# Optimization experiments

Measured on AMD Instinct MI355X. Metric: run time of the kernel, lower is better.

The kernel has to match this reference:

```python
import jax, jax.numpy as jnp
import numpy as np
import math

EMBED_DIM = 1024
N_HEADS = 16
HEAD_DIM = EMBED_DIM // N_HEADS
B, N = 2, 2048


def setup_inputs() -> dict:
    key = jax.random.key(0)
    k1, k2, k3 = jax.random.split(key, 3)
    x = jax.random.normal(k1, (B, N, EMBED_DIM), dtype=jnp.float32)
    # Per-head Linear(D, 3*head_dim), stacked over heads. PyTorch Linear init scale ~1/sqrt(fan_in).
    bound = 1.0 / math.sqrt(EMBED_DIM)
    Wkqv = jax.random.uniform(k2, (N_HEADS, EMBED_DIM, 3 * HEAD_DIM), dtype=jnp.float32, minval=-bound, maxval=bound)
    bkqv = jax.random.uniform(k3, (N_HEADS, 3 * HEAD_DIM), dtype=jnp.float32, minval=-bound, maxval=bound)
    return {"x": x, "Wkqv": Wkqv, "bkqv": bkqv}


def reference(x, Wkqv, bkqv):
    Bx, Nx, D = x.shape
    hd = Wkqv.shape[-1] // 3
    # all heads at once: [B, H, N, 3*hd]
    proj = jnp.einsum('bnd,hdf->bhnf', x, Wkqv) + bkqv[None, :, None, :]
    # torch.split order in the original is (k, q, v)
    k, q, v = jnp.split(proj, 3, axis=-1)
    # scores = q @ k^T / sqrt(head_dim)   [B, H, N, N]
    scores = jnp.einsum('bhqd,bhkd->bhqk', q, k) / math.sqrt(hd)
    causal = jnp.tril(jnp.ones((Nx, Nx), dtype=bool))
    scores = jnp.where(causal[None, None, :, :], scores, -jnp.inf)
    attn = jax.nn.softmax(scores, axis=-1)
    out = jnp.einsum('bhqk,bhkd->bhqd', attn, v)  # [B, H, N, hd]
    # concat heads -> [B, N, D]  (forward() passes no out_matrix, so no output projection)
    return out.transpose(0, 2, 1, 3).reshape(Bx, Nx, D)
```

## Files before the change

kernel.cpp:

```cpp
#include <hip/hip_runtime.h>
#include <math.h>

typedef float f32x4 __attribute__((ext_vector_type(4)));
typedef __bf16 bf16x8 __attribute__((ext_vector_type(8)));

#define MFMA16(a, b, c) __builtin_amdgcn_mfma_f32_16x16x32_bf16((a), (b), (c), 0, 0, 0)

constexpr int Bsz = 2, Nseq = 2048, Dm = 1024, Hh = 16, HDim = 64, F3 = 192;
constexpr int Mrows = Bsz * Nseq;
constexpr int NC = Hh * F3;
constexpr float QSCALE = 0.125f * 1.4426950408889634f;

__device__ inline void load_lds16(const void* g, void* l) {
    __builtin_amdgcn_global_load_lds((const __attribute__((address_space(1))) void*)g,
                                     (__attribute__((address_space(3))) void*)l, 16, 0, 0);
}

__global__ __launch_bounds__(256) void conv_x_kernel(const float* __restrict__ x,
                                                     __bf16* __restrict__ xb) {
    int i = blockIdx.x * 256 + threadIdx.x;
    const float4* xv = reinterpret_cast<const float4*>(x);
    float4 a = xv[2 * i];
    float4 b = xv[2 * i + 1];
    bf16x8 o = {(__bf16)a.x, (__bf16)a.y, (__bf16)a.z, (__bf16)a.w,
                (__bf16)b.x, (__bf16)b.y, (__bf16)b.z, (__bf16)b.w};
    *reinterpret_cast<bf16x8*>(xb + 8 * i) = o;
}

__global__ __launch_bounds__(256) void conv_w_kernel(const float* __restrict__ w,
                                                     __bf16* __restrict__ wt) {
    __shared__ __bf16 tile[32][66];
    int h = blockIdx.z, d0 = blockIdx.x * 32, c0 = blockIdx.y * 64;
    for (int i = threadIdx.x; i < 32 * 64; i += 256) {
        int di = i >> 6, cj = i & 63;
        tile[di][cj] = (__bf16)w[(size_t)(h * Dm + d0 + di) * F3 + c0 + cj];
    }
    __syncthreads();
    for (int i = threadIdx.x; i < 32 * 64; i += 256) {
        int ci = i >> 5, dj = i & 31;
        wt[(size_t)(h * F3 + c0 + ci) * Dm + d0 + dj] = tile[dj][ci];
    }
}

__global__ __launch_bounds__(512, 2) void gemm_proj(const __bf16* __restrict__ xb,
                                                    const __bf16* __restrict__ wt,
                                                    const float* __restrict__ bias,
                                                    __bf16* __restrict__ kbuf,
                                                    __bf16* __restrict__ qbuf,
                                                    __bf16* __restrict__ vt) {
    __shared__ __align__(16) __bf16 Ab[2][256 * 64];
    __shared__ __align__(16) __bf16 Bb[2][256 * 64];

    int flat = blockIdx.x;
    int swz = (flat & 7) * 24 + (flat >> 3);
    int bm = swz / 12, bn = swz % 12;
    int r0 = bm * 256, n0 = bn * 256;

    int w = threadIdx.x >> 6, lane = threadIdx.x & 63;
    int col = lane & 15, quad = lane >> 4;
    int wm = w >> 2, wn = w & 3;

    f32x4 acc[8][4] = {};

    auto stage = [&](int kt, int s) {
        int rbase = w * 32;
        int rl = lane >> 3;
        int cg = ((lane & 7) ^ rl) * 8;
#pragma unroll
        for (int i = 0; i < 4; i++) {
            int row = rbase + i * 8 + rl;
            load_lds16(xb + (size_t)(r0 + row) * Dm + kt * 64 + cg,
                       &Ab[s][(rbase + i * 8) * 64]);
            load_lds16(wt + (size_t)(n0 + row) * Dm + kt * 64 + cg,
                       &Bb[s][(rbase + i * 8) * 64]);
        }
    };

    stage(0, 0);
    stage(1, 1);

    for (int j = 0; j < 16; j++) {
        int s = j & 1;
        if (j < 15) asm volatile("s_waitcnt vmcnt(8)" ::: "memory");
        else        asm volatile("s_waitcnt vmcnt(0)" ::: "memory");
        __builtin_amdgcn_s_barrier();
        asm volatile("" ::: "memory");

#pragma unroll
        for (int ks = 0; ks < 2; ks++) {
            int cq = ks * 4 + quad;
            bf16x8 af[8], bfr[4];
#pragma unroll
            for (int mt = 0; mt < 8; mt++) {
                int row = wm * 128 + mt * 16 + col;
                af[mt] = *reinterpret_cast<const bf16x8*>(
                    &Ab[s][row * 64 + ((cq ^ (row & 7)) * 8)]);
            }
#pragma unroll
            for (int nt = 0; nt < 4; nt++) {
                int row = wn * 64 + nt * 16 + col;
                bfr[nt] = *reinterpret_cast<const bf16x8*>(
                    &Bb[s][row * 64 + ((cq ^ (row & 7)) * 8)]);
            }
            __builtin_amdgcn_s_setprio(1);
#pragma unroll
            for (int mt = 0; mt < 8; mt++)
#pragma unroll
                for (int nt = 0; nt < 4; nt++)
                    acc[mt][nt] = MFMA16(af[mt], bfr[nt], acc[mt][nt]);
            __builtin_amdgcn_s_setprio(0);
        }

        asm volatile("" ::: "memory");
        __builtin_amdgcn_s_barrier();
        asm volatile("" ::: "memory");
        if (j + 2 < 16) stage(j + 2, s);
    }

#pragma unroll
    for (int nt = 0; nt < 4; nt++) {
        int g = n0 + wn * 64 + nt * 16 + col;
        int h = g / F3, c = g - h * F3;
        float bv = bias[g];
        bool isq = (c >= 64 && c < 128), isv = (c >= 128);
        int cd = c & 63;
#pragma unroll
        for (int mt = 0; mt < 8; mt++) {
#pragma unroll
            for (int rg = 0; rg < 4; rg++) {
                int r = r0 + wm * 128 + mt * 16 + quad * 4 + rg;
                int b = r >> 11, n = r & (Nseq - 1);
                float v = acc[mt][nt][rg] + bv;
                if (isq) v *= QSCALE;
                size_t bh = (size_t)(b * Hh + h);
                if (isv) vt[(bh * HDim + cd) * Nseq + n] = (__bf16)v;
                else ((isq) ? qbuf : kbuf)[(bh * Nseq + n) * HDim + cd] = (__bf16)v;
            }
        }
    }
}

__global__ __launch_bounds__(256) void proj_small(const float* __restrict__ x,
                                                  const __bf16* __restrict__ wt,
                                                  const float* __restrict__ bias,
                                                  __bf16* __restrict__ kbuf,
                                                  __bf16* __restrict__ qbuf,
                                                  __bf16* __restrict__ vt) {
    int h = blockIdx.y;
    int wave = threadIdx.x >> 6, lane = threadIdx.x & 63;
    int col = lane & 15, quad = lane >> 4;
    int r0 = blockIdx.x * 128 + wave * 32;

    f32x4 acc[12][2] = {};
    const float* xr0 = x + (size_t)(r0 + col) * Dm + quad * 8;
    const float* xr1 = xr0 + 16 * Dm;
    const __bf16* wbase = wt + (size_t)(h * F3 + col) * Dm + quad * 8;

    for (int k0 = 0; k0 < Dm; k0 += 32) {
        float4 a0lo = *reinterpret_cast<const float4*>(xr0 + k0);
        float4 a0hi = *reinterpret_cast<const float4*>(xr0 + k0 + 4);
        float4 a1lo = *reinterpret_cast<const float4*>(xr1 + k0);
        float4 a1hi = *reinterpret_cast<const float4*>(xr1 + k0 + 4);
        bf16x8 a0 = {(__bf16)a0lo.x, (__bf16)a0lo.y, (__bf16)a0lo.z, (__bf16)a0lo.w,
                     (__bf16)a0hi.x, (__bf16)a0hi.y, (__bf16)a0hi.z, (__bf16)a0hi.w};
        bf16x8 a1 = {(__bf16)a1lo.x, (__bf16)a1lo.y, (__bf16)a1lo.z, (__bf16)a1lo.w,
                     (__bf16)a1hi.x, (__bf16)a1hi.y, (__bf16)a1hi.z, (__bf16)a1hi.w};
#pragma unroll
        for (int ct = 0; ct < 12; ct++) {
            bf16x8 bf = *reinterpret_cast<const bf16x8*>(wbase + ct * 16 * Dm + k0);
            acc[ct][0] = MFMA16(a0, bf, acc[ct][0]);
            acc[ct][1] = MFMA16(a1, bf, acc[ct][1]);
        }
    }
#pragma unroll
    for (int ct = 0; ct < 12; ct++) {
        int c = ct * 16 + col;
        float bv = bias[h * F3 + c];
        int cd = c & 63;
        bool isq = (c >= 64 && c < 128), isv = (c >= 128);
#pragma unroll
        for (int rt = 0; rt < 2; rt++) {
#pragma unroll
            for (int rg = 0; rg < 4; rg++) {
                int r = r0 + rt * 16 + quad * 4 + rg;
                int b = r >> 11, n = r & (Nseq - 1);
                float v = acc[ct][rt][rg] + bv;
                if (isq) v *= QSCALE;
                size_t bh = (size_t)(b * Hh + h);
                if (isv) vt[(bh * HDim + cd) * Nseq + n] = (__bf16)v;
                else ((isq) ? qbuf : kbuf)[(bh * Nseq + n) * HDim + cd] = (__bf16)v;
            }
        }
    }
}

__global__ __launch_bounds__(512) void attn_kernel(const __bf16* __restrict__ qbuf,
                                                   const __bf16* __restrict__ kbuf,
                                                   const __bf16* __restrict__ vt,
                                                   float* __restrict__ out) {
    __shared__ __align__(16) __bf16 Kb[64 * 64];
    __shared__ __align__(16) __bf16 Vb[64 * 64];
    __shared__ __align__(16) __bf16 plds[8][16][72];
    int bh = blockIdx.x;
    int b = bh >> 4, h = bh & 15;
    int pair = blockIdx.y;
    int wave = threadIdx.x >> 6, lane = threadIdx.x & 63;
    int col = lane & 15, quad = lane >> 4;
    int tile = (wave < 4) ? pair : (31 - pair);
    int q0 = tile * 64 + (wave & 3) * 16;

    const __bf16* qbase = qbuf + (size_t)bh * Nseq * HDim;
    const __bf16* kbase = kbuf + (size_t)bh * Nseq * HDim;
    const __bf16* vbase = vt + (size_t)bh * HDim * Nseq;

    bf16x8 aq0 = *reinterpret_cast<const bf16x8*>(qbase + (q0 + col) * HDim + quad * 8);
    bf16x8 aq1 = *reinterpret_cast<const bf16x8*>(qbase + (q0 + col) * HDim + quad * 8 + 32);

    f32x4 o[4] = {};
    float lsum[4] = {0.f, 0.f, 0.f, 0.f};

    int mb = q0 & ~63;
    int loop_end = 2048 - 64 * pair;

    int srow = threadIdx.x >> 3;
    int schunk = (threadIdx.x & 7) ^ (srow & 7);
    const __bf16* ksrc0 = kbase + srow * HDim + schunk * 8;
    const __bf16* vsrc0 = vbase + (size_t)srow * Nseq + schunk * 8;
    __bf16* kdst = Kb + wave * 512;
    __bf16* vdst = Vb + wave * 512;

    int sw0 = ((quad ^ (col & 7)) * 8);
    int sw1 = (((quad + 4) ^ (col & 7)) * 8);

    for (int kb = 0; kb < loop_end; kb += 64) {
        __syncthreads();
        load_lds16(ksrc0 + kb * HDim, kdst);
        load_lds16(vsrc0 + kb, vdst);
        __syncthreads();

        if (kb <= mb) {
            bool masked = (kb == mb);
            f32x4 z = {};
            f32x4 s[4];
#pragma unroll
            for (int g = 0; g < 4; g++) {
                const __bf16* krow = Kb + (col + 16 * g) * 64;
                bf16x8 k0 = *reinterpret_cast<const bf16x8*>(krow + sw0);
                bf16x8 k1 = *reinterpret_cast<const bf16x8*>(krow + sw1);
                s[g] = MFMA16(aq0, k0, z);
                s[g] = MFMA16(aq1, k1, s[g]);
            }
            if (masked) {
#pragma unroll
                for (int g = 0; g < 4; g++) {
#pragma unroll
                    for (int r = 0; r < 4; r++) {
                        int qi = q0 + quad * 4 + r;
                        float p = (kb + col + 16 * g <= qi) ? exp2f(s[g][r]) : 0.f;
                        lsum[r] += p;
                        plds[wave][quad * 4 + r][col + 16 * g] = (__bf16)p;
                    }
                }
            } else {
#pragma unroll
                for (int g = 0; g < 4; g++) {
#pragma unroll
                    for (int r = 0; r < 4; r++) {
                        float p = exp2f(s[g][r]);
                        lsum[r] += p;
                        plds[wave][quad * 4 + r][col + 16 * g] = (__bf16)p;
                    }
                }
            }
            bf16x8 pa0 = *reinterpret_cast<const bf16x8*>(&plds[wave][col][quad * 8]);
            bf16x8 pa1 = *reinterpret_cast<const bf16x8*>(&plds[wave][col][32 + quad * 8]);
#pragma unroll
            for (int nt = 0; nt < 4; nt++) {
                const __bf16* vrow = Vb + (col + 16 * nt) * 64;
                bf16x8 v0 = *reinterpret_cast<const bf16x8*>(vrow + sw0);
                bf16x8 v1 = *reinterpret_cast<const bf16x8*>(vrow + sw1);
                o[nt] = MFMA16(pa0, v0, o[nt]);
                o[nt] = MFMA16(pa1, v1, o[nt]);
            }
        }
    }

    float linv[4];
#pragma unroll
    for (int r = 0; r < 4; r++) {
        float s = lsum[r];
        s += __shfl_xor(s, 1);
        s += __shfl_xor(s, 2);
        s += __shfl_xor(s, 4);
        s += __shfl_xor(s, 8);
        linv[r] = 1.f / s;
    }
#pragma unroll
    for (int nt = 0; nt < 4; nt++) {
#pragma unroll
        for (int r = 0; r < 4; r++) {
            int qi = q0 + quad * 4 + r;
            out[((size_t)(b * Nseq + qi)) * Dm + h * HDim + nt * 16 + col] = o[nt][r] * linv[r];
        }
    }
}

extern "C" void kernel_launch(void* const* d_in, const int* in_sizes, int n_in,
                              void* d_out, int out_size, void* d_ws, size_t ws_size,
                              hipStream_t stream) {
    const float* x = nullptr;
    const float* w = nullptr;
    const float* bias = nullptr;
    for (int i = 0; i < n_in; i++) {
        if (in_sizes[i] == Mrows * Dm) x = (const float*)d_in[i];
        else if (in_sizes[i] == Hh * Dm * F3) w = (const float*)d_in[i];
        else if (in_sizes[i] == Hh * F3) bias = (const float*)d_in[i];
    }
    float* outp = (float*)d_out;

    char* ws = (char*)d_ws;
    __bf16* wt = (__bf16*)(ws);
    __bf16* kbuf = (__bf16*)(ws + 6291456);
    __bf16* qbuf = (__bf16*)(ws + 6291456 + 8388608);
    __bf16* vt = (__bf16*)(ws + 6291456 + 2 * 8388608);
    __bf16* xb = (__bf16*)(ws + 6291456 + 3 * 8388608);

    conv_w_kernel<<<dim3(Dm / 32, F3 / 64, Hh), 256, 0, stream>>>(w, wt);
    if (ws_size >= (size_t)(6291456 + 4 * 8388608)) {
        conv_x_kernel<<<Mrows * Dm / (8 * 256), 256, 0, stream>>>(x, xb);
        gemm_proj<<<dim3(Mrows / 256 * (NC / 256)), 512, 0, stream>>>(xb, wt, bias, kbuf, qbuf, vt);
    } else {
        proj_small<<<dim3(Mrows / 128, Hh), 256, 0, stream>>>(x, wt, bias, kbuf, qbuf, vt);
    }
    attn_kernel<<<dim3(32, 16), 512, 0, stream>>>(qbuf, kbuf, vt, outp);
}
```

Baseline: 169.6 us.

## Restructure QKV projection GEMM main loop into quarter-tile interleaved load/compute schedule

Replaces the simple double-buffered K-loop of the QKV projection GEMM with a finer-grained 8-phase schedule. The 256x256 tile is split into half-tiles of A and B, and their global-to-LDS loads are interleaved between quarter-tile MFMA blocks, with barriers around each block. The goal is to overlap memory traffic with MFMA work more evenly and to reduce register pressure by holding fewer fragments at once. The cost is many more barriers per iteration and more complex buffer-reuse ordering, which could cause stalls or races if the waitcnt accounting is wrong.

```diff
diff --git a/kernel.cpp b/kernel.cpp
--- a/kernel.cpp
+++ b/kernel.cpp
@@ -15,6 +15,10 @@
     __builtin_amdgcn_global_load_lds((const __attribute__((address_space(1))) void*)g,
                                      (__attribute__((address_space(3))) void*)l, 16, 0, 0);
 }
+
+#define FENCE asm volatile("" ::: "memory")
+#define BARRIER do { FENCE; __builtin_amdgcn_s_barrier(); FENCE; } while (0)
+#define WAIT6 asm volatile("s_waitcnt vmcnt(6)" ::: "memory")
 
 __global__ __launch_bounds__(256) void conv_x_kernel(const float* __restrict__ x,
                                                      __bf16* __restrict__ xb) {
@@ -61,60 +65,105 @@
     int wm = w >> 2, wn = w & 3;
 
     f32x4 acc[8][4] = {};
-
-    auto stage = [&](int kt, int s) {
-        int rbase = w * 32;
+    bf16x8 af[2][4];
+    bf16x8 bfr[2][2];
+
+    auto stageA = [&](int t, int s, int h) {
         int rl = lane >> 3;
-        int cg = ((lane & 7) ^ rl) * 8;
-#pragma unroll
-        for (int i = 0; i < 4; i++) {
-            int row = rbase + i * 8 + rl;
-            load_lds16(xb + (size_t)(r0 + row) * Dm + kt * 64 + cg,
-                       &Ab[s][(rbase + i * 8) * 64]);
-            load_lds16(wt + (size_t)(n0 + row) * Dm + kt * 64 + cg,
-                       &Bb[s][(rbase + i * 8) * 64]);
-        }
-    };
-
-    stage(0, 0);
-    stage(1, 1);
-
-    for (int j = 0; j < 16; j++) {
-        int s = j & 1;
-        if (j < 15) asm volatile("s_waitcnt vmcnt(8)" ::: "memory");
-        else        asm volatile("s_waitcnt vmcnt(0)" ::: "memory");
-        __builtin_amdgcn_s_barrier();
-        asm volatile("" ::: "memory");
-
-#pragma unroll
-        for (int ks = 0; ks < 2; ks++) {
-            int cq = ks * 4 + quad;
-            bf16x8 af[8], bfr[4];
-#pragma unroll
-            for (int mt = 0; mt < 8; mt++) {
-                int row = wm * 128 + mt * 16 + col;
-                af[mt] = *reinterpret_cast<const bf16x8*>(
-                    &Ab[s][row * 64 + ((cq ^ (row & 7)) * 8)]);
-            }
-#pragma unroll
-            for (int nt = 0; nt < 4; nt++) {
-                int row = wn * 64 + nt * 16 + col;
-                bfr[nt] = *reinterpret_cast<const bf16x8*>(
-                    &Bb[s][row * 64 + ((cq ^ (row & 7)) * 8)]);
-            }
-            __builtin_amdgcn_s_setprio(1);
-#pragma unroll
-            for (int mt = 0; mt < 8; mt++)
-#pragma unroll
-                for (int nt = 0; nt < 4; nt++)
-                    acc[mt][nt] = MFMA16(af[mt], bfr[nt], acc[mt][nt]);
-            __builtin_amdgcn_s_setprio(0);
-        }
-
-        asm volatile("" ::: "memory");
-        __builtin_amdgcn_s_barrier();
-        asm volatile("" ::: "memory");
-        if (j + 2 < 16) stage(j + 2, s);
+        int cg = (lane & 7) ^ rl;
+#pragma unroll
+        for (int r = 0; r < 2; r++) {
+            int rowb = r * 128 + h * 64 + w * 8;
+            load_lds16(xb + (size_t)(r0 + rowb + rl) * Dm + t * 64 + cg * 8,
+                       &Ab[s][rowb * 64]);
+        }
+    };
+    auto stageB = [&](int t, int s, int h) {
+        int rl = lane >> 3;
+        int cg = (lane & 7) ^ rl;
+#pragma unroll
+        for (int r = 0; r < 2; r++) {
+            int rowb = ((w >> 2) + r * 2) * 64 + h * 32 + (w & 3) * 8;
+            load_lds16(wt + (size_t)(n0 + rowb + rl) * Dm + t * 64 + cg * 8,
+                       &Bb[s][rowb * 64]);
+        }
+    };
+
+    auto readA = [&](int s, int mh) {
+#pragma unroll
+        for (int ks = 0; ks < 2; ks++)
+#pragma unroll
+            for (int mt = 0; mt < 4; mt++) {
+                int row = wm * 128 + mh * 64 + mt * 16 + col;
+                af[ks][mt] = *reinterpret_cast<const bf16x8*>(
+                    &Ab[s][row * 64 + (((ks * 4 + quad) ^ (row & 7)) * 8)]);
+            }
+    };
+    auto readB = [&](int s, int nh) {
+#pragma unroll
+        for (int ks = 0; ks < 2; ks++)
+#pragma unroll
+            for (int nt = 0; nt < 2; nt++) {
+                int row = wn * 64 + nh * 32 + nt * 16 + col;
+                bfr[ks][nt] = *reinterpret_cast<const bf16x8*>(
+                    &Bb[s][row * 64 + (((ks * 4 + quad) ^ (row & 7)) * 8)]);
+            }
+    };
+    auto mfmaQ = [&](int mh, int nh) {
+        __builtin_amdgcn_s_setprio(1);
+#pragma unroll
+        for (int ks = 0; ks < 2; ks++)
+#pragma unroll
+            for (int mt = 0; mt < 4; mt++)
+#pragma unroll
+                for (int nt = 0; nt < 2; nt++)
+                    acc[mh * 4 + mt][nh * 2 + nt] =
+                        MFMA16(af[ks][mt], bfr[ks][nt], acc[mh * 4 + mt][nh * 2 + nt]);
+        __builtin_amdgcn_s_setprio(0);
+    };
+
+    stageA(0, 0, 0); stageB(0, 0, 0); stageA(0, 0, 1); stageB(0, 0, 1);
+    stageA(1, 1, 0);
+    stageB(1, 1, 0); stageA(1, 1, 1);
+    WAIT6;
+    BARRIER;
+
+    for (int i = 0; i < 8; i++) {
+        int t0 = 2 * i;
+        int t2 = t0 + 2; if (t2 > 15) t2 = 15;
+        int t3 = t0 + 3; if (t3 > 15) t3 = 15;
+
+        readA(0, 0); readB(0, 0);
+        stageB(t0 + 1, 1, 1);
+        BARRIER; mfmaQ(0, 0); BARRIER;
+
+        readB(0, 1);
+        stageA(t2, 0, 0);
+        BARRIER; mfmaQ(0, 1); BARRIER;
+
+        readA(0, 1); readB(0, 0);
+        BARRIER; mfmaQ(1, 0); BARRIER;
+
+        readB(0, 1);
+        stageB(t2, 0, 0); stageA(t2, 0, 1);
+        WAIT6;
+        BARRIER; mfmaQ(1, 1); BARRIER;
+
+        readA(1, 0); readB(1, 0);
+        stageB(t2, 0, 1);
+        BARRIER; mfmaQ(0, 0); BARRIER;
+
+        readB(1, 1);
+        stageA(t3, 1, 0);
+        BARRIER; mfmaQ(0, 1); BARRIER;
+
+        readA(1, 1); readB(1, 0);
+        BARRIER; mfmaQ(1, 0); BARRIER;
+
+        readB(1, 1);
+        stageB(t3, 1, 0); stageA(t3, 1, 1);
+        WAIT6;
+        BARRIER; mfmaQ(1, 1); BARRIER;
     }
 
 #pragma unroll
```

After: 172.0 us. About the same (+1.4%).

## Retile projection GEMM to 256x192 and double-buffer attention K/V with per-tile blocks

Applied to the files above, without the earlier changes.

The projection GEMM moves from 256x256 to 256x192 output tiles, giving 256 blocks instead of 192 to fill the CUs better. The attention kernel stops pairing a short and a long query tile in one 512-thread block. It now launches one 256-thread block per 64-row query tile, heaviest tiles first, and double-buffers K/V loads into LDS so the next block's load overlaps compute. The risks are more blocks, load imbalance across the causal triangle, and lower MFMA reuse per B-fragment in the GEMM.

```diff
diff --git a/kernel.cpp b/kernel.cpp
--- a/kernel.cpp
+++ b/kernel.cpp
@@ -15,6 +15,9 @@
     __builtin_amdgcn_global_load_lds((const __attribute__((address_space(1))) void*)g,
                                      (__attribute__((address_space(3))) void*)l, 16, 0, 0);
 }
+
+#define FENCE asm volatile("" ::: "memory")
+#define BARRIER do { FENCE; __builtin_amdgcn_s_barrier(); FENCE; } while (0)
 
 __global__ __launch_bounds__(256) void conv_x_kernel(const float* __restrict__ x,
                                                      __bf16* __restrict__ xb) {
@@ -49,30 +52,34 @@
                                                     __bf16* __restrict__ qbuf,
                                                     __bf16* __restrict__ vt) {
     __shared__ __align__(16) __bf16 Ab[2][256 * 64];
-    __shared__ __align__(16) __bf16 Bb[2][256 * 64];
+    __shared__ __align__(16) __bf16 Bb[2][192 * 64];
 
     int flat = blockIdx.x;
-    int swz = (flat & 7) * 24 + (flat >> 3);
-    int bm = swz / 12, bn = swz % 12;
-    int r0 = bm * 256, n0 = bn * 256;
+    int swz = (flat & 7) * 32 + (flat >> 3);
+    int bm = swz >> 4, bn = swz & 15;
+    int r0 = bm * 256, n0 = bn * 192;
 
     int w = threadIdx.x >> 6, lane = threadIdx.x & 63;
     int col = lane & 15, quad = lane >> 4;
     int wm = w >> 2, wn = w & 3;
 
-    f32x4 acc[8][4] = {};
-
-    auto stage = [&](int kt, int s) {
-        int rbase = w * 32;
-        int rl = lane >> 3;
-        int cg = ((lane & 7) ^ rl) * 8;
+    f32x4 acc[8][3] = {};
+
+    int rl = lane >> 3;
+    int cg = ((lane & 7) ^ rl) * 8;
+
+    auto stage = [&](int t, int s) {
 #pragma unroll
         for (int i = 0; i < 4; i++) {
-            int row = rbase + i * 8 + rl;
-            load_lds16(xb + (size_t)(r0 + row) * Dm + kt * 64 + cg,
-                       &Ab[s][(rbase + i * 8) * 64]);
-            load_lds16(wt + (size_t)(n0 + row) * Dm + kt * 64 + cg,
-                       &Bb[s][(rbase + i * 8) * 64]);
+            int rowb = w * 32 + i * 8;
+            load_lds16(xb + (size_t)(r0 + rowb + rl) * Dm + t * 64 + cg,
+                       &Ab[s][rowb * 64]);
+        }
+#pragma unroll
+        for (int i = 0; i < 3; i++) {
+            int rowb = w * 24 + i * 8;
+            load_lds16(wt + (size_t)(n0 + rowb + rl) * Dm + t * 64 + cg,
+                       &Bb[s][rowb * 64]);
         }
     };
 
@@ -81,15 +88,14 @@
 
     for (int j = 0; j < 16; j++) {
         int s = j & 1;
-        if (j < 15) asm volatile("s_waitcnt vmcnt(8)" ::: "memory");
+        if (j < 15) asm volatile("s_waitcnt vmcnt(7)" ::: "memory");
         else        asm volatile("s_waitcnt vmcnt(0)" ::: "memory");
-        __builtin_amdgcn_s_barrier();
-        asm volatile("" ::: "memory");
+        BARRIER;
 
 #pragma unroll
         for (int ks = 0; ks < 2; ks++) {
             int cq = ks * 4 + quad;
-            bf16x8 af[8], bfr[4];
+            bf16x8 af[8], bfr[3];
 #pragma unroll
             for (int mt = 0; mt < 8; mt++) {
                 int row = wm * 128 + mt * 16 + col;
@@ -97,8 +103,8 @@
                     &Ab[s][row * 64 + ((cq ^ (row & 7)) * 8)]);
             }
 #pragma unroll
-            for (int nt = 0; nt < 4; nt++) {
-                int row = wn * 64 + nt * 16 + col;
+            for (int nt = 0; nt < 3; nt++) {
+                int row = wn * 48 + nt * 16 + col;
                 bfr[nt] = *reinterpret_cast<const bf16x8*>(
                     &Bb[s][row * 64 + ((cq ^ (row & 7)) * 8)]);
             }
@@ -106,20 +112,18 @@
 #pragma unroll
             for (int mt = 0; mt < 8; mt++)
 #pragma unroll
-                for (int nt = 0; nt < 4; nt++)
+                for (int nt = 0; nt < 3; nt++)
                     acc[mt][nt] = MFMA16(af[mt], bfr[nt], acc[mt][nt]);
             __builtin_amdgcn_s_setprio(0);
         }
 
-        asm volatile("" ::: "memory");
-        __builtin_amdgcn_s_barrier();
-        asm volatile("" ::: "memory");
+        BARRIER;
         if (j + 2 < 16) stage(j + 2, s);
     }
 
 #pragma unroll
-    for (int nt = 0; nt < 4; nt++) {
-        int g = n0 + wn * 64 + nt * 16 + col;
+    for (int nt = 0; nt < 3; nt++) {
+        int g = n0 + wn * 48 + nt * 16 + col;
         int h = g / F3, c = g - h * F3;
         float bv = bias[g];
         bool isq = (c >= 64 && c < 128), isv = (c >= 128);
@@ -194,20 +198,19 @@
     }
 }
 
-__global__ __launch_bounds__(512) void attn_kernel(const __bf16* __restrict__ qbuf,
+__global__ __launch_bounds__(256) void attn_kernel(const __bf16* __restrict__ qbuf,
                                                    const __bf16* __restrict__ kbuf,
                                                    const __bf16* __restrict__ vt,
                                                    float* __restrict__ out) {
-    __shared__ __align__(16) __bf16 Kb[64 * 64];
-    __shared__ __align__(16) __bf16 Vb[64 * 64];
-    __shared__ __align__(16) __bf16 plds[8][16][72];
+    __shared__ __align__(16) __bf16 Kb[2][64 * 64];
+    __shared__ __align__(16) __bf16 Vb[2][64 * 64];
+    __shared__ __align__(16) __bf16 plds[4][16][72];
     int bh = blockIdx.x;
     int b = bh >> 4, h = bh & 15;
-    int pair = blockIdx.y;
+    int tile = 31 - blockIdx.y;
     int wave = threadIdx.x >> 6, lane = threadIdx.x & 63;
     int col = lane & 15, quad = lane >> 4;
-    int tile = (wave < 4) ? pair : (31 - pair);
-    int q0 = tile * 64 + (wave & 3) * 16;
+    int q0 = tile * 64 + wave * 16;
 
     const __bf16* qbase = qbuf + (size_t)bh * Nseq * HDim;
     const __bf16* kbase = kbuf + (size_t)bh * Nseq * HDim;
@@ -219,81 +222,97 @@
     f32x4 o[4] = {};
     float lsum[4] = {0.f, 0.f, 0.f, 0.f};
 
-    int mb = q0 & ~63;
-    int loop_end = 2048 - 64 * pair;
-
-    int srow = threadIdx.x >> 3;
-    int schunk = (threadIdx.x & 7) ^ (srow & 7);
-    const __bf16* ksrc0 = kbase + srow * HDim + schunk * 8;
-    const __bf16* vsrc0 = vbase + (size_t)srow * Nseq + schunk * 8;
-    __bf16* kdst = Kb + wave * 512;
-    __bf16* vdst = Vb + wave * 512;
+    int mb = tile * 64;
+    int loop_end = mb + 64;
+
+    int rl = lane >> 3;
+    int srow0 = wave * 16 + rl;
+    int srow1 = wave * 16 + 8 + rl;
+    int sc = (lane & 7) ^ rl;
+    const __bf16* ksrc0 = kbase + srow0 * HDim + sc * 8;
+    const __bf16* ksrc1 = kbase + srow1 * HDim + sc * 8;
+    const __bf16* vsrc0 = vbase + (size_t)srow0 * Nseq + sc * 8;
+    const __bf16* vsrc1 = vbase + (size_t)srow1 * Nseq + sc * 8;
+    int d0 = wave * 1024, d1 = wave * 1024 + 512;
 
     int sw0 = ((quad ^ (col & 7)) * 8);
     int sw1 = (((quad + 4) ^ (col & 7)) * 8);
 
+    load_lds16(ksrc0, &Kb[0][d0]);
+    load_lds16(ksrc1, &Kb[0][d1]);
+    load_lds16(vsrc0, &Vb[0][d0]);
+    load_lds16(vsrc1, &Vb[0][d1]);
+    FENCE;
+
+    int s = 0;
     for (int kb = 0; kb < loop_end; kb += 64) {
-        __syncthreads();
-        load_lds16(ksrc0 + kb * HDim, kdst);
-        load_lds16(vsrc0 + kb, vdst);
-        __syncthreads();
-
-        if (kb <= mb) {
-            bool masked = (kb == mb);
-            f32x4 z = {};
-            f32x4 s[4];
+        asm volatile("s_waitcnt vmcnt(0)" ::: "memory");
+        BARRIER;
+        int nkb = kb + 64;
+        if (nkb < loop_end) {
+            load_lds16(ksrc0 + nkb * HDim, &Kb[s ^ 1][d0]);
+            load_lds16(ksrc1 + nkb * HDim, &Kb[s ^ 1][d1]);
+            load_lds16(vsrc0 + nkb, &Vb[s ^ 1][d0]);
+            load_lds16(vsrc1 + nkb, &Vb[s ^ 1][d1]);
+        }
+
+        bool masked = (kb == mb);
+        const __bf16* Kcur = Kb[s];
+        const __bf16* Vcur = Vb[s];
+        f32x4 z = {};
+        f32x4 sc4[4];
+#pragma unroll
+        for (int g = 0; g < 4; g++) {
+            const __bf16* krow = Kcur + (col + 16 * g) * 64;
+            bf16x8 k0 = *reinterpret_cast<const bf16x8*>(krow + sw0);
+            bf16x8 k1 = *reinterpret_cast<const bf16x8*>(krow + sw1);
+            sc4[g] = MFMA16(aq0, k0, z);
+            sc4[g] = MFMA16(aq1, k1, sc4[g]);
+        }
+        if (masked) {
 #pragma unroll
             for (int g = 0; g < 4; g++) {
-                const __bf16* krow = Kb + (col + 16 * g) * 64;
-                bf16x8 k0 = *reinterpret_cast<const bf16x8*>(krow + sw0);
-                bf16x8 k1 = *reinterpret_cast<const bf16x8*>(krow + sw1);
-                s[g] = MFMA16(aq0, k0, z);
-                s[g] = MFMA16(aq1, k1, s[g]);
-            }
-            if (masked) {
-#pragma unroll
-                for (int g = 0; g < 4; g++) {
-#pragma unroll
-                    for (int r = 0; r < 4; r++) {
-                        int qi = q0 + quad * 4 + r;
-                        float p = (kb + col + 16 * g <= qi) ? exp2f(s[g][r]) : 0.f;
-                        lsum[r] += p;
-                        plds[wave][quad * 4 + r][col + 16 * g] = (__bf16)p;
-                    }
+#pragma unroll
+                for (int r = 0; r < 4; r++) {
+                    int qi = q0 + quad * 4 + r;
+                    float p = (kb + col + 16 * g <= qi) ? exp2f(sc4[g][r]) : 0.f;
+                    lsum[r] += p;
+                    plds[wave][quad * 4 + r][col + 16 * g] = (__bf16)p;
                 }
-            } else {
-#pragma unroll
-                for (int g = 0; g < 4; g++) {
-#pragma unroll
-                    for (int r = 0; r < 4; r++) {
-                        float p = exp2f(s[g][r]);
-                        lsum[r] += p;
-                        plds[wave][quad * 4 + r][col + 16 * g] = (__bf16)p;
-                    }
+            }
+        } else {
+#pragma unroll
+            for (int g = 0; g < 4; g++) {
+#pragma unroll
+                for (int r = 0; r < 4; r++) {
+                    float p = exp2f(sc4[g][r]);
+                    lsum[r] += p;
+                    plds[wave][quad * 4 + r][col + 16 * g] = (__bf16)p;
                 }
             }
-            bf16x8 pa0 = *reinterpret_cast<const bf16x8*>(&plds[wave][col][quad * 8]);
-            bf16x8 pa1 = *reinterpret_cast<const bf16x8*>(&plds[wave][col][32 + quad * 8]);
-#pragma unroll
-            for (int nt = 0; nt < 4; nt++) {
-                const __bf16* vrow = Vb + (col + 16 * nt) * 64;
-                bf16x8 v0 = *reinterpret_cast<const bf16x8*>(vrow + sw0);
-                bf16x8 v1 = *reinterpret_cast<const bf16x8*>(vrow + sw1);
-                o[nt] = MFMA16(pa0, v0, o[nt]);
-                o[nt] = MFMA16(pa1, v1, o[nt]);
-            }
-        }
+        }
+        bf16x8 pa0 = *reinterpret_cast<const bf16x8*>(&plds[wave][col][quad * 8]);
+        bf16x8 pa1 = *reinterpret_cast<const bf16x8*>(&plds[wave][col][32 + quad * 8]);
+#pragma unroll
+        for (int nt = 0; nt < 4; nt++) {
+            const __bf16* vrow = Vcur + (col + 16 * nt) * 64;
+            bf16x8 v0 = *reinterpret_cast<const bf16x8*>(vrow + sw0);
+            bf16x8 v1 = *reinterpret_cast<const bf16x8*>(vrow + sw1);
+            o[nt] = MFMA16(pa0, v0, o[nt]);
+            o[nt] = MFMA16(pa1, v1, o[nt]);
+        }
+        s ^= 1;
     }
 
     float linv[4];
 #pragma unroll
     for (int r = 0; r < 4; r++) {
-        float s = lsum[r];
-        s += __shfl_xor(s, 1);
-        s += __shfl_xor(s, 2);
-        s += __shfl_xor(s, 4);
-        s += __shfl_xor(s, 8);
-        linv[r] = 1.f / s;
+        float t = lsum[r];
+        t += __shfl_xor(t, 1);
+        t += __shfl_xor(t, 2);
+        t += __shfl_xor(t, 4);
+        t += __shfl_xor(t, 8);
+        linv[r] = 1.f / t;
     }
 #pragma unroll
     for (int nt = 0; nt < 4; nt++) {
@@ -328,9 +347,9 @@
     conv_w_kernel<<<dim3(Dm / 32, F3 / 64, Hh), 256, 0, stream>>>(w, wt);
     if (ws_size >= (size_t)(6291456 + 4 * 8388608)) {
         conv_x_kernel<<<Mrows * Dm / (8 * 256), 256, 0, stream>>>(x, xb);
-        gemm_proj<<<dim3(Mrows / 256 * (NC / 256)), 512, 0, stream>>>(xb, wt, bias, kbuf, qbuf, vt);
+        gemm_proj<<<dim3((Mrows / 256) * (NC / 192)), 512, 0, stream>>>(xb, wt, bias, kbuf, qbuf, vt);
     } else {
         proj_small<<<dim3(Mrows / 128, Hh), 256, 0, stream>>>(x, wt, bias, kbuf, qbuf, vt);
     }
-    attn_kernel<<<dim3(32, 16), 512, 0, stream>>>(qbuf, kbuf, vt, outp);
-}
+    attn_kernel<<<dim3(32, 32), 256, 0, stream>>>(qbuf, kbuf, vt, outp);
+}
```

Measured after the change: 159.1 us. 6.2% less time.
